# Kernel tuning notes

Measured on AMD Instinct MI355X. Metric: run time of the kernel, lower is better.

The kernel has to match this reference:

```python
import jax, jax.numpy as jnp
import numpy as np
from jax import lax

TIME_STEPS = 49          # saves at t = 1..49
STEPS_PER_SAVE = 100     # dt = 0.01 -> 100 Euler steps per unit time
DT = 0.01
B = 8192                 # Monte-Carlo batch
EPS = 1e-7


def setup_inputs() -> dict:
    key = jax.random.key(0)
    condition = jax.random.uniform(key, (B, 4), dtype=jnp.float32)
    return {"condition": condition, "seed": 0}


def _simulate(inf, rec, mr, vol, noise):
    # inf/rec/mr/vol: [B]; noise: [TIME_STEPS, STEPS_PER_SAVE, B] ~ N(0, DT)
    r0_mean = inf / rec
    s0 = jnp.full_like(inf, 0.99)
    i0 = jnp.full_like(inf, 0.01)
    r0_ = jnp.zeros_like(inf)
    y0 = (s0, i0, r0_, r0_mean)  # y0[3] = infection_rate / recovery_rate

    def euler_step(carry, dw):  # dw: [B]
        s, i, r, r0 = carry
        newly_infected = r0 * rec * s
        newly_recovered = rec * i
        s_n = s - DT * newly_infected
        i_n = i + DT * (newly_infected - newly_recovered)
        r_n = r + DT * newly_recovered
        # drift mean-reversion + diffusion scaled by sqrt(|r0|)
        r0_n = r0 + DT * mr * (r0_mean - r0) + jnp.sqrt(jnp.abs(r0)) * vol * dw
        return (s_n, i_n, r_n, r0_n), None

    def save_block(carry, dws):  # dws: [STEPS_PER_SAVE, B]
        carry, _ = lax.scan(euler_step, carry, dws)
        return carry, carry[1]  # save infected fraction at integer times

    _, infected = lax.scan(save_block, y0, noise)  # [TIME_STEPS, B]
    return jnp.nan_to_num(infected, nan=0.0, posinf=0.0, neginf=0.0).T  # [B, T]


def _summarize(x, u):
    # x: [B, TIME_STEPS] infected trajectory, u: [B] uniform
    x = jnp.clip(x, 1e-5)
    max_ = x.max(axis=1)
    max_at = (jnp.argmax(x, axis=1).astype(x.dtype) + u) / TIME_STEPS
    vol = jnp.std(jnp.diff(jnp.log(x), axis=1), axis=1)
    s_loc = jnp.array([0.38, 0.21, 0.14], dtype=x.dtype)
    s_scale = jnp.array([0.14, 0.12, 0.03], dtype=x.dtype)
    s = jnp.stack([max_, max_at, vol], axis=-1)  # [B, 3]
    return (s - s_loc) / s_scale


def reference(condition, seed):
    p = jnp.clip(condition, EPS, 1.0 - EPS)  # [B, 4]
    inf, rec, mr, vol = p[:, 0], p[:, 1], p[:, 2], p[:, 3]
    k_noise, k_u = jax.random.split(jax.random.key(seed))
    noise = jax.random.normal(
        k_noise, (TIME_STEPS, STEPS_PER_SAVE, B), dtype=jnp.float32
    ) * jnp.sqrt(jnp.float32(DT))
    infected = _simulate(inf, rec, mr, vol, noise)  # [B, TIME_STEPS]
    u = jax.random.uniform(k_u, (B,), dtype=jnp.float32)
    return _summarize(infected, u)  # [B, 3]
```

## Files before the change

### kernel.cpp

```cpp
#include <hip/hip_runtime.h>
#include <cstdint>

#pragma clang fp contract(off)

#define TSAVES 49
#define SPSAVE 100
#define NB 8192
#define TRAJ 32
#define GENW 14
#define NITER 51

typedef float f32x4 __attribute__((ext_vector_type(4)));

__device__ __forceinline__ uint32_t rotl32(uint32_t v, int d) {
  return __builtin_rotateleft32(v, (uint32_t)d);
}

__device__ __forceinline__ void tf2x32(uint32_t k0, uint32_t k1,
                                       uint32_t x0, uint32_t x1,
                                       uint32_t& o0, uint32_t& o1) {
  uint32_t ks2 = k0 ^ k1 ^ 0x1BD11BDAu;
#define TF_ROUND(r) { x0 += x1; x1 = rotl32(x1, r); x1 ^= x0; }
  x0 += k0; x1 += k1;
  TF_ROUND(13) TF_ROUND(15) TF_ROUND(26) TF_ROUND(6)
  x0 += k1; x1 += ks2 + 1u;
  TF_ROUND(17) TF_ROUND(29) TF_ROUND(16) TF_ROUND(24)
  x0 += ks2; x1 += k0 + 2u;
  TF_ROUND(13) TF_ROUND(15) TF_ROUND(26) TF_ROUND(6)
  x0 += k0; x1 += k1 + 3u;
  TF_ROUND(17) TF_ROUND(29) TF_ROUND(16) TF_ROUND(24)
  x0 += k1; x1 += ks2 + 4u;
  TF_ROUND(13) TF_ROUND(15) TF_ROUND(26) TF_ROUND(6)
  x0 += ks2; x1 += k0 + 5u;
#undef TF_ROUND
  o0 = x0; o1 = x1;
}

__device__ __forceinline__ void derive_keys(int seed, uint32_t& kn0, uint32_t& kn1,
                                            uint32_t& ku0, uint32_t& ku1) {
  uint64_t sv = (uint64_t)(int64_t)seed;
  uint32_t k0 = (uint32_t)(sv >> 32);
  uint32_t k1 = (uint32_t)(sv & 0xffffffffULL);
  tf2x32(k0, k1, 0u, 0u, kn0, kn1);
  tf2x32(k0, k1, 0u, 1u, ku0, ku1);
}

__device__ __forceinline__ uint32_t rand_bits32(uint32_t k0, uint32_t k1, uint32_t n) {
  uint32_t y0, y1;
  tf2x32(k0, k1, 0u, n, y0, y1);
  return y0 ^ y1;
}

__device__ __forceinline__ float bits_to_eu(uint32_t bits) {
#pragma clang fp contract(fast)
  float u01 = __uint_as_float((bits >> 9) | 0x3f800000u) - 1.0f;
  float u = u01 * 2.0f + (-0.99999994f);
  u = fmaxf(-0.99999994f, u);
  float omu2 = 1.0f - u * u;
  float w = -(__builtin_amdgcn_logf(omu2) * 0.6931472f);
  float p;
  if (w < 5.0f) {
    float z = w - 2.5f;
    p = 2.81022636e-08f;
    p = 3.43273939e-07f + p * z;
    p = -3.5233877e-06f + p * z;
    p = -4.39150654e-06f + p * z;
    p = 0.00021858087f + p * z;
    p = -0.00125372503f + p * z;
    p = -0.00417768164f + p * z;
    p = 0.246640727f + p * z;
    p = 1.50140941f + p * z;
  } else {
    float z = __builtin_amdgcn_sqrtf(w) - 3.0f;
    p = -0.000200214257f;
    p = 0.000100950558f + p * z;
    p = 0.00134934322f + p * z;
    p = -0.00367342844f + p * z;
    p = 0.00573950773f + p * z;
    p = -0.0076224613f + p * z;
    p = 0.00943887047f + p * z;
    p = 1.00167406f + p * z;
    p = 2.83297682f + p * z;
  }
  return p * u;
}

__device__ __forceinline__ float clip_param(float x) {
  return fminf(0.99999988f, fmaxf(1e-07f, x));
}

__global__ __launch_bounds__(1024) void fused_kernel(const float* __restrict__ cond,
                                                     const int* __restrict__ seedp,
                                                     float* __restrict__ out) {
  __shared__ f32x4 nbuf[2][25][TRAJ];
  __shared__ f32x4 rbuf[2][25][TRAJ];
  const int tid = threadIdx.x;
  const int lane = tid & 63;
  const int wv = tid >> 6;
  const int bbase = blockIdx.x * TRAJ;
  const int tr = lane & 31;
  const int h = lane >> 5;
  const int b = bbase + tr;

  uint32_t kn0, kn1, ku0, ku1;
  derive_keys(seedp[0], kn0, kn1, ku0, ku1);

  float pinf = clip_param(cond[b * 4 + 0]);
  float prec = clip_param(cond[b * 4 + 1]);
  float pmr  = clip_param(cond[b * 4 + 2]);
  float pvol = clip_param(cond[b * 4 + 3]);
  const float r0m  = pinf / prec;
  const float dtmr = 0.01f * pmr;
  const float c4 = 1.0f - dtmr;
  const float a4 = dtmr * r0m;
  const float c2 = 0.01f * prec;
  const float c3 = 1.0f - c2;
  const float c3p4 = (c3 * c3) * (c3 * c3);
  const float cpv = 0.14142136f * pvol;

  float r0 = r0m;
  float s = 0.99f, i = 0.01f, r0in = r0m;
  float best = -1.0f; int bi = 0;
  float plg = 0.0f, sd = 0.0f, sd2 = 0.0f;

  for (int g = 0; g < NITER; ++g) {
    if (wv < GENW) {
      if (g <= 48) {
        const uint32_t nbase = (uint32_t)(g * SPSAVE) * (uint32_t)NB + (uint32_t)b;
        float* nb = (float*)&nbuf[g & 1][0][0];
#pragma unroll
        for (int k = 0; k < 4; ++k) {
          const int id = wv + GENW * k;
          if (id < 50) {
            const int c = id >> 1;
            const int e = ((id & 1) << 1) | h;
            uint32_t n = nbase + (uint32_t)(4 * c + e) * (uint32_t)NB;
            float eu = bits_to_eu(rand_bits32(kn0, kn1, n));
            nb[(c * 32 + tr) * 4 + e] = eu * cpv;
          }
        }
      }
    } else if (wv == GENW) {
      if (g >= 1 && g <= 49) {
        const int src = (g - 1) & 1;
        f32x4 vd = nbuf[src][0][tr];
#pragma unroll
        for (int c = 0; c < 25; ++c) {
          f32x4 vdn = (c < 24) ? nbuf[src][c + 1][tr] : vd;
          f32x4 w;
#pragma unroll
          for (int e = 0; e < 4; ++e) {
            float sq  = __builtin_amdgcn_sqrtf(fabsf(r0));
            float r0h = fmaf(c4, r0, a4);
            r0 = fmaf(sq, vd[e], r0h);
            w[e] = r0;
          }
          rbuf[src][c][tr] = w;
          vd = vdn;
        }
      }
    } else {
      if (g >= 2) {
        const int t = g - 2;
        const int src = g & 1;
        f32x4 rv = rbuf[src][0][tr];
#pragma unroll
        for (int c = 0; c < 25; ++c) {
          f32x4 rvn = (c < 24) ? rbuf[src][c + 1][tr] : rv;
          float rs0 = r0in * s;  s = fmaf(-c2, rs0, s);
          float rs1 = rv[0] * s; s = fmaf(-c2, rs1, s);
          float rs2 = rv[1] * s; s = fmaf(-c2, rs2, s);
          float rs3 = rv[2] * s; s = fmaf(-c2, rs3, s);
          float hh = fmaf(c3, rs0, rs1);
          hh = fmaf(c3, hh, rs2);
          hh = fmaf(c3, hh, rs3);
          i = fmaf(c3p4, i, c2 * hh);
          r0in = rv[3];
          rv = rvn;
        }
        float v = i;
        if (!isfinite(v)) v = 0.0f;
        float x = fmaxf(v, 1e-05f);
        if (x > best) { best = x; bi = t; }
        float lg = __builtin_amdgcn_logf(x) * 0.6931472f;
        if (t > 0) { float d = lg - plg; sd += d; sd2 += d * d; }
        plg = lg;
      }
    }
    __syncthreads();
  }

  if (wv == GENW + 1 && lane < TRAJ) {
    uint32_t ub = rand_bits32(ku0, ku1, (uint32_t)b);
    float u = __uint_as_float((ub >> 9) | 0x3f800000u) - 1.0f;
    u = fmaxf(0.0f, u);
    float maxat = ((float)bi + u) / 49.0f;
    float mean = sd / 48.0f;
    float var = sd2 / 48.0f - mean * mean;
    float stdv = sqrtf(fmaxf(var, 0.0f));
    out[b * 3 + 0] = (best  - 0.38f) / 0.14f;
    out[b * 3 + 1] = (maxat - 0.21f) / 0.12f;
    out[b * 3 + 2] = (stdv  - 0.14f) / 0.03f;
  }
}

extern "C" void kernel_launch(void* const* d_in, const int* in_sizes, int n_in,
                              void* d_out, int out_size, void* d_ws, size_t ws_size,
                              hipStream_t stream) {
  const float* cond = (const float*)d_in[0];
  const int* seedp = (const int*)d_in[1];
  float* out = (float*)d_out;
  (void)d_ws; (void)ws_size;
  fused_kernel<<<NB / TRAJ, 1024, 0, stream>>>(cond, seedp, out);
}
```

Before: 158.7 us.

## Replace per-stage block barriers with LDS flag-based producer/consumer handoff

Drops the lockstep loop with a __syncthreads every stage and gives the generator waves, the r0 wave and the SIR wave each their own loop. They coordinate through volatile shared-memory progress flags and sleep-polling. Each stage can now run ahead as far as double buffering allows, so fast waves no longer wait on the slowest one every iteration. The cost is spin-polling overhead and reliance on LDS memory ordering through __threadfence_block.

Result: faster. 150.2 us (-5.4%).

```diff
diff --git a/kernel.cpp b/kernel.cpp
--- a/kernel.cpp
+++ b/kernel.cpp
@@ -8,7 +8,6 @@
 #define NB 8192
 #define TRAJ 32
 #define GENW 14
-#define NITER 51
 
 typedef float f32x4 __attribute__((ext_vector_type(4)));
 
@@ -94,6 +93,8 @@
                                                      float* __restrict__ out) {
   __shared__ f32x4 nbuf[2][25][TRAJ];
   __shared__ f32x4 rbuf[2][25][TRAJ];
+  __shared__ int flags[GENW + 2];
+
   const int tid = threadIdx.x;
   const int lane = tid & 63;
   const int wv = tid >> 6;
@@ -101,6 +102,10 @@
   const int tr = lane & 31;
   const int h = lane >> 5;
   const int b = bbase + tr;
+
+  if (tid < GENW + 2) flags[tid] = 0;
+  __syncthreads();
+  volatile int* vflags = flags;
 
   uint32_t kn0, kn1, ku0, ku1;
   derive_keys(seedp[0], kn0, kn1, ku0, ku1);
@@ -118,89 +123,105 @@
   const float c3p4 = (c3 * c3) * (c3 * c3);
   const float cpv = 0.14142136f * pvol;
 
-  float r0 = r0m;
-  float s = 0.99f, i = 0.01f, r0in = r0m;
-  float best = -1.0f; int bi = 0;
-  float plg = 0.0f, sd = 0.0f, sd2 = 0.0f;
-
-  for (int g = 0; g < NITER; ++g) {
-    if (wv < GENW) {
-      if (g <= 48) {
-        const uint32_t nbase = (uint32_t)(g * SPSAVE) * (uint32_t)NB + (uint32_t)b;
-        float* nb = (float*)&nbuf[g & 1][0][0];
-#pragma unroll
-        for (int k = 0; k < 4; ++k) {
-          const int id = wv + GENW * k;
-          if (id < 50) {
-            const int c = id >> 1;
-            const int e = ((id & 1) << 1) | h;
-            uint32_t n = nbase + (uint32_t)(4 * c + e) * (uint32_t)NB;
-            float eu = bits_to_eu(rand_bits32(kn0, kn1, n));
-            nb[(c * 32 + tr) * 4 + e] = eu * cpv;
-          }
+  if (wv < GENW) {
+    for (int g = 0; g <= 48; ++g) {
+      if (g >= 2) {
+        while (vflags[GENW] < g - 1) __builtin_amdgcn_s_sleep(1);
+      }
+      const uint32_t nbase = (uint32_t)(g * SPSAVE) * (uint32_t)NB + (uint32_t)b;
+      float* nb = (float*)&nbuf[g & 1][0][0];
+#pragma unroll
+      for (int k = 0; k < 4; ++k) {
+        const int id = wv + GENW * k;
+        if (id < 50) {
+          const int c = id >> 1;
+          const int e = ((id & 1) << 1) | h;
+          uint32_t n = nbase + (uint32_t)(4 * c + e) * (uint32_t)NB;
+          float eu = bits_to_eu(rand_bits32(kn0, kn1, n));
+          nb[(c * 32 + tr) * 4 + e] = eu * cpv;
         }
       }
-    } else if (wv == GENW) {
-      if (g >= 1 && g <= 49) {
-        const int src = (g - 1) & 1;
-        f32x4 vd = nbuf[src][0][tr];
-#pragma unroll
-        for (int c = 0; c < 25; ++c) {
-          f32x4 vdn = (c < 24) ? nbuf[src][c + 1][tr] : vd;
-          f32x4 w;
-#pragma unroll
-          for (int e = 0; e < 4; ++e) {
-            float sq  = __builtin_amdgcn_sqrtf(fabsf(r0));
-            float r0h = fmaf(c4, r0, a4);
-            r0 = fmaf(sq, vd[e], r0h);
-            w[e] = r0;
-          }
-          rbuf[src][c][tr] = w;
-          vd = vdn;
+      __threadfence_block();
+      if (lane == 0) vflags[wv] = g + 1;
+    }
+  } else if (wv == GENW) {
+    float r0 = r0m;
+    for (int g = 0; g <= 48; ++g) {
+      for (;;) {
+        int mn = vflags[0];
+#pragma unroll
+        for (int w = 1; w < GENW; ++w) { int v = vflags[w]; mn = (v < mn) ? v : mn; }
+        if (mn >= g + 1) break;
+        __builtin_amdgcn_s_sleep(1);
+      }
+      if (g >= 2) {
+        while (vflags[GENW + 1] < g - 1) __builtin_amdgcn_s_sleep(1);
+      }
+      __threadfence_block();
+      const int src = g & 1;
+      f32x4 vd = nbuf[src][0][tr];
+#pragma unroll
+      for (int c = 0; c < 25; ++c) {
+        f32x4 vdn = (c < 24) ? nbuf[src][c + 1][tr] : vd;
+        f32x4 w;
+#pragma unroll
+        for (int e = 0; e < 4; ++e) {
+          float sq  = __builtin_amdgcn_sqrtf(fabsf(r0));
+          float r0h = fmaf(c4, r0, a4);
+          r0 = fmaf(sq, vd[e], r0h);
+          w[e] = r0;
         }
-      }
-    } else {
-      if (g >= 2) {
-        const int t = g - 2;
-        const int src = g & 1;
-        f32x4 rv = rbuf[src][0][tr];
-#pragma unroll
-        for (int c = 0; c < 25; ++c) {
-          f32x4 rvn = (c < 24) ? rbuf[src][c + 1][tr] : rv;
-          float rs0 = r0in * s;  s = fmaf(-c2, rs0, s);
-          float rs1 = rv[0] * s; s = fmaf(-c2, rs1, s);
-          float rs2 = rv[1] * s; s = fmaf(-c2, rs2, s);
-          float rs3 = rv[2] * s; s = fmaf(-c2, rs3, s);
-          float hh = fmaf(c3, rs0, rs1);
-          hh = fmaf(c3, hh, rs2);
-          hh = fmaf(c3, hh, rs3);
-          i = fmaf(c3p4, i, c2 * hh);
-          r0in = rv[3];
-          rv = rvn;
-        }
-        float v = i;
-        if (!isfinite(v)) v = 0.0f;
-        float x = fmaxf(v, 1e-05f);
-        if (x > best) { best = x; bi = t; }
-        float lg = __builtin_amdgcn_logf(x) * 0.6931472f;
-        if (t > 0) { float d = lg - plg; sd += d; sd2 += d * d; }
-        plg = lg;
-      }
-    }
-    __syncthreads();
-  }
-
-  if (wv == GENW + 1 && lane < TRAJ) {
-    uint32_t ub = rand_bits32(ku0, ku1, (uint32_t)b);
-    float u = __uint_as_float((ub >> 9) | 0x3f800000u) - 1.0f;
-    u = fmaxf(0.0f, u);
-    float maxat = ((float)bi + u) / 49.0f;
-    float mean = sd / 48.0f;
-    float var = sd2 / 48.0f - mean * mean;
-    float stdv = sqrtf(fmaxf(var, 0.0f));
-    out[b * 3 + 0] = (best  - 0.38f) / 0.14f;
-    out[b * 3 + 1] = (maxat - 0.21f) / 0.12f;
-    out[b * 3 + 2] = (stdv  - 0.14f) / 0.03f;
+        rbuf[src][c][tr] = w;
+        vd = vdn;
+      }
+      __threadfence_block();
+      if (lane == 0) vflags[GENW] = g + 1;
+    }
+  } else {
+    float s = 0.99f, i = 0.01f, r0in = r0m;
+    float best = -1.0f; int bi = 0;
+    float plg = 0.0f, sd = 0.0f, sd2 = 0.0f;
+    for (int g = 0; g <= 48; ++g) {
+      while (vflags[GENW] < g + 1) __builtin_amdgcn_s_sleep(1);
+      __threadfence_block();
+      const int src = g & 1;
+      f32x4 rv = rbuf[src][0][tr];
+#pragma unroll
+      for (int c = 0; c < 25; ++c) {
+        f32x4 rvn = (c < 24) ? rbuf[src][c + 1][tr] : rv;
+        float rs0 = r0in * s;  s = fmaf(-c2, rs0, s);
+        float rs1 = rv[0] * s; s = fmaf(-c2, rs1, s);
+        float rs2 = rv[1] * s; s = fmaf(-c2, rs2, s);
+        float rs3 = rv[2] * s; s = fmaf(-c2, rs3, s);
+        float hh = fmaf(c3, rs0, rs1);
+        hh = fmaf(c3, hh, rs2);
+        hh = fmaf(c3, hh, rs3);
+        i = fmaf(c3p4, i, c2 * hh);
+        r0in = rv[3];
+        rv = rvn;
+      }
+      float v = i;
+      if (!isfinite(v)) v = 0.0f;
+      float x = fmaxf(v, 1e-05f);
+      if (x > best) { best = x; bi = g; }
+      float lg = __builtin_amdgcn_logf(x) * 0.6931472f;
+      if (g > 0) { float d = lg - plg; sd += d; sd2 += d * d; }
+      plg = lg;
+      __threadfence_block();
+      if (lane == 0) vflags[GENW + 1] = g + 1;
+    }
+    if (lane < TRAJ) {
+      uint32_t ub = rand_bits32(ku0, ku1, (uint32_t)b);
+      float u = __uint_as_float((ub >> 9) | 0x3f800000u) - 1.0f;
+      u = fmaxf(0.0f, u);
+      float maxat = ((float)bi + u) / 49.0f;
+      float mean = sd / 48.0f;
+      float var = sd2 / 48.0f - mean * mean;
+      float stdv = sqrtf(fmaxf(var, 0.0f));
+      out[b * 3 + 0] = (best  - 0.38f) / 0.14f;
+      out[b * 3 + 1] = (maxat - 0.21f) / 0.12f;
+      out[b * 3 + 2] = (stdv  - 0.14f) / 0.03f;
+    }
   }
 }
 
```
